# Performance work log

Hardware: AMD Instinct MI355X
Metric: run time of the kernel (lower is better)

Reference implementation:

```python
import jax, jax.numpy as jnp
import numpy as np

FP4_VALUES = jnp.array([0.0, 0.5, 1.0, 1.5, 2.0, 3.0, 4.0, 6.0,
                        -0.0, -0.5, -1.0, -1.5, -2.0, -3.0, -4.0, -6.0], dtype=jnp.float32)
ALPHA = 1.702
LIMIT = 7.0


def convert_moe_packed_tensors(blocks, scales):
    """Dequantize MXFP4: blocks [E, R, G, 16] packed nibbles, scales [E, R, G] biased exponents.
    Returns [E, G*32, R] fp32 (transposed like the torch reference)."""
    lo = FP4_VALUES[blocks & 0x0F]          # even output positions
    hi = FP4_VALUES[(blocks >> 4) & 0x0F]   # odd output positions
    vals = jnp.stack([lo, hi], axis=-1).reshape(*blocks.shape[:-1], 32)  # [E,R,G,32] interleaved
    scale = jnp.exp2((scales - 127).astype(jnp.float32))                 # 2**(s-127)
    w = vals * scale[..., None]
    E, R = blocks.shape[0], blocks.shape[1]
    return w.reshape(E, R, -1).transpose(0, 2, 1)  # [E, G*32, R]


def setup_inputs() -> dict:
    key = jax.random.key(0)
    ks = jax.random.split(key, 8)
    E, H, I = 8, 2880, 2880
    B, S = 1, 1024
    hidden_states = jax.random.normal(ks[0], (B, S, H), dtype=jnp.float32)
    routing_weights = jax.random.uniform(ks[1], (B * S, E), dtype=jnp.float32)
    gate_up_proj_blocks = jax.random.randint(ks[2], (E, 2 * I, H // 32, 16), 0, 256, dtype=jnp.int32)
    gate_up_proj_scales = jax.random.randint(ks[3], (E, 2 * I, H // 32), 118, 130, dtype=jnp.int32)
    gate_up_proj_bias = jax.random.normal(ks[4], (E, 2 * I), dtype=jnp.float32)
    down_proj_blocks = jax.random.randint(ks[5], (E, H, I // 32, 16), 0, 256, dtype=jnp.int32)
    down_proj_scales = jax.random.randint(ks[6], (E, H, I // 32), 118, 130, dtype=jnp.int32)
    down_proj_bias = jax.random.normal(ks[7], (E, H), dtype=jnp.float32)
    return {
        "hidden_states": hidden_states,
        "routing_weights": routing_weights,
        "gate_up_proj_blocks": gate_up_proj_blocks,
        "gate_up_proj_scales": gate_up_proj_scales,
        "gate_up_proj_bias": gate_up_proj_bias,
        "down_proj_blocks": down_proj_blocks,
        "down_proj_scales": down_proj_scales,
        "down_proj_bias": down_proj_bias,
    }


def reference(hidden_states, routing_weights, gate_up_proj_blocks, gate_up_proj_scales,
              gate_up_proj_bias, down_proj_blocks, down_proj_scales, down_proj_bias):
    B, S, H = hidden_states.shape
    gate_up_proj = convert_moe_packed_tensors(gate_up_proj_blocks, gate_up_proj_scales)  # [E, H, 2I]
    down_proj = convert_moe_packed_tensors(down_proj_blocks, down_proj_scales)           # [E, I, H]
    x = hidden_states.reshape(-1, H)                                                     # [T, H]
    # dense all-expert GLU MLP
    gate_up = jnp.einsum('th,ehf->etf', x, gate_up_proj) + gate_up_proj_bias[:, None, :]  # [E, T, 2I]
    gate = jnp.minimum(gate_up[..., ::2], LIMIT)
    up = jnp.clip(gate_up[..., 1::2], -LIMIT, LIMIT)
    glu = gate * jax.nn.sigmoid(gate * ALPHA)
    nxt = jnp.einsum('eti,eih->eth', (up + 1.0) * glu, down_proj) + down_proj_bias[:, None, :]  # [E, T, H]
    nxt = nxt * routing_weights.T[:, :, None]   # weight each expert's output per token
    out = nxt.sum(axis=0).reshape(B, S, H)
    return out
```

## Files before the change

### kernel.cpp

```cpp
#include <hip/hip_runtime.h>
#include <cstdint>


typedef float  floatx4 __attribute__((ext_vector_type(4)));
typedef __bf16 bf16x8  __attribute__((ext_vector_type(8)));

#define E8   8
#define Hdim 2880
#define Idim 2880
#define Ttok 1024
#define R1   5760
#define Gg   90
#define K2   (E8 * Idim)

__device__ __forceinline__ void load_lds16(const void* gptr, void* lptr) {
  __builtin_amdgcn_global_load_lds(
      (const __attribute__((address_space(1))) uint32_t*)gptr,
      (__attribute__((address_space(3))) uint32_t*)lptr, 16, 0, 0);
}

__device__ __forceinline__ uint32_t f2bf(float f) {
  uint32_t u = __float_as_uint(f);
  return (u + 0x7FFFu + ((u >> 16) & 1u)) >> 16;
}

__device__ __forceinline__ uint32_t perm(uint32_t hi, uint32_t lo, uint32_t sel) {
  return __builtin_amdgcn_perm(hi, lo, sel);
}

struct DqLut { uint32_t Ll, Lh, Hl, Hh; };

__device__ __forceinline__ DqLut make_lut(int s) {
  uint32_t A  = ((uint32_t)(s - 127) << 7) & 0xFFFFu;
  uint32_t e1 = (0x3F00u + A) & 0xFFFFu, e2 = (0x3F80u + A) & 0xFFFFu;
  uint32_t e3 = (0x3FC0u + A) & 0xFFFFu, e4 = (0x4000u + A) & 0xFFFFu;
  uint32_t e5 = (0x4040u + A) & 0xFFFFu, e6 = (0x4080u + A) & 0xFFFFu;
  uint32_t e7 = (0x40C0u + A) & 0xFFFFu;
  uint32_t B01 = e1 << 16, B23 = e2 | (e3 << 16);
  uint32_t B45 = e4 | (e5 << 16), B67 = e6 | (e7 << 16);
  DqLut L;
  L.Ll = perm(B23, B01, 0x06040200u);
  L.Hl = perm(B23, B01, 0x07050301u);
  L.Lh = perm(B67, B45, 0x06040200u);
  L.Hh = perm(B67, B45, 0x07050301u);
  return L;
}

__device__ __forceinline__ uint4 dq8(const DqLut& L, int4 wr) {
  uint32_t p = perm((uint32_t)wr.y, (uint32_t)wr.x, 0x04000400u);
  uint32_t q = perm((uint32_t)wr.w, (uint32_t)wr.z, 0x04000400u);
  uint32_t w = perm(q, p, 0x05040100u);
  uint32_t ilo = w & 0x07070707u;
  uint32_t ihi = (w >> 4) & 0x07070707u;
  uint32_t Llo = perm(L.Lh, L.Ll, ilo);
  uint32_t Hlo = perm(L.Hh, L.Hl, ilo) | ((w << 4) & 0x80808080u);
  uint32_t Lhi = perm(L.Lh, L.Ll, ihi);
  uint32_t Hhi = perm(L.Hh, L.Hl, ihi) | (w & 0x80808080u);
  uint32_t t0 = perm(Hlo, Llo, 0x05010400u);
  uint32_t t1 = perm(Hlo, Llo, 0x07030602u);
  uint32_t t2 = perm(Hhi, Lhi, 0x05010400u);
  uint32_t t3 = perm(Hhi, Lhi, 0x07030602u);
  uint4 o;
  o.x = perm(t2, t0, 0x05040100u);
  o.y = perm(t2, t0, 0x07060302u);
  o.z = perm(t3, t1, 0x05040100u);
  o.w = perm(t3, t1, 0x07060302u);
  return o;
}

__global__ void cvt_x_kernel(const float* __restrict__ x, uint16_t* __restrict__ xb, int n) {
  int i = (blockIdx.x * 256 + threadIdx.x) * 4;
  if (i >= n) return;
  float4 v = *(const float4*)(x + i);
  ushort4 o = make_ushort4((uint16_t)f2bf(v.x), (uint16_t)f2bf(v.y),
                           (uint16_t)f2bf(v.z), (uint16_t)f2bf(v.w));
  *(ushort4*)(xb + i) = o;
}

__global__ void dq_w_kernel(const int* __restrict__ blocks, const int* __restrict__ scales,
                            uint16_t* __restrict__ wd) {
  size_t g = (size_t)blockIdx.x * 256 + threadIdx.x;
  const int4* bp = (const int4*)(blocks + g * 16);
  int4 w0 = bp[0], w1 = bp[1], w2 = bp[2], w3 = bp[3];
  DqLut L = make_lut(scales[g]);
  uint4* op = (uint4*)(wd + g * 32);
  op[0] = dq8(L, w0); op[1] = dq8(L, w1); op[2] = dq8(L, w2); op[3] = dq8(L, w3);
}

__global__ void dq_w2t_kernel(const int* __restrict__ blocks, const int* __restrict__ scales,
                              uint16_t* __restrict__ wt) {
  size_t g = (size_t)blockIdx.x * 256 + threadIdx.x;
  int e  = (int)(g / ((size_t)Hdim * Gg));
  int rm = (int)(g % ((size_t)Hdim * Gg));
  int h  = rm / Gg;
  int ig = rm % Gg;
  const int4* bp = (const int4*)(blocks + g * 16);
  int4 w0 = bp[0], w1 = bp[1], w2 = bp[2], w3 = bp[3];
  DqLut L = make_lut(scales[g]);
  uint4* op = (uint4*)(wt + ((size_t)h * E8 + e) * Idim + (size_t)ig * 32);
  op[0] = dq8(L, w0); op[1] = dq8(L, w1); op[2] = dq8(L, w2); op[3] = dq8(L, w3);
}

__global__ void bias_init_kernel(const float* __restrict__ rw, const float* __restrict__ bias,
                                 float* __restrict__ out) {
  int t  = blockIdx.y;
  int h4 = (blockIdx.x * 256 + threadIdx.x) * 4;
  if (h4 >= Hdim) return;
  float4 s = make_float4(0.f, 0.f, 0.f, 0.f);
  #pragma unroll
  for (int e = 0; e < E8; ++e) {
    float w = rw[t * E8 + e];
    float4 b = *(const float4*)(bias + (size_t)e * Hdim + h4);
    s.x += w * b.x; s.y += w * b.y; s.z += w * b.z; s.w += w * b.w;
  }
  *(float4*)(out + (size_t)t * Hdim + h4) = s;
}

__global__ __launch_bounds__(256) void gemm1_pd_kernel(
    const uint16_t* __restrict__ xb, const uint16_t* __restrict__ w1d,
    const float* __restrict__ bias, const float* __restrict__ rw,
    uint16_t* __restrict__ act) {
  __shared__ uint16_t sA[128 * 64];
  __shared__ uint16_t sB[128 * 64];
  const int tid  = threadIdx.x;
  const int lane = tid & 63, wv = tid >> 6;
  const int wx = wv & 1, wy = wv >> 1;
  const int col = lane & 15, quad = lane >> 4;
  const int e  = blockIdx.z;
  const int t0 = blockIdx.x * 128;
  const int i0 = blockIdx.y * 64;

  floatx4 acc[4][4] = {};

  const uint16_t* aSrc[4];
  const uint16_t* bSrc[4];
  uint16_t* aDst[4];
  uint16_t* bDst[4];
  #pragma unroll
  for (int q = 0; q < 4; ++q) {
    int L = wv * 256 + q * 64 + lane;
    int row = L >> 3;
    int c = (L & 7) ^ (row & 7);
    aSrc[q] = xb + (size_t)(t0 + row) * Hdim + c * 8;
    aDst[q] = &sA[(size_t)(wv * 256 + q * 64) * 8];
    int orig = 2 * (((row >> 6) << 5) + (row & 31)) + ((row >> 5) & 1);
    bSrc[q] = w1d + ((size_t)e * R1 + 2 * i0 + orig) * Hdim + c * 8;
    bDst[q] = &sB[(size_t)(wv * 256 + q * 64) * 8];
  }

  for (int kt = 0; kt < 45; ++kt) {
    __syncthreads();
    const int k0 = kt * 64;
    #pragma unroll
    for (int q = 0; q < 4; ++q) load_lds16(aSrc[q] + k0, aDst[q]);
    #pragma unroll
    for (int q = 0; q < 4; ++q) load_lds16(bSrc[q] + k0, bDst[q]);
    __syncthreads();
    #pragma unroll
    for (int ks = 0; ks < 2; ++ks) {
      bf16x8 af[4], bfr[4];
      #pragma unroll
      for (int fm = 0; fm < 4; ++fm) {
        int row = wy * 64 + fm * 16 + col;
        int c = ((ks << 2) | quad) ^ (row & 7);
        af[fm] = *(const bf16x8*)&sA[row * 64 + c * 8];
      }
      #pragma unroll
      for (int fn = 0; fn < 4; ++fn) {
        int row = wx * 64 + fn * 16 + col;
        int c = ((ks << 2) | quad) ^ (row & 7);
        bfr[fn] = *(const bf16x8*)&sB[row * 64 + c * 8];
      }
      #pragma unroll
      for (int fm = 0; fm < 4; ++fm)
        #pragma unroll
        for (int fn = 0; fn < 4; ++fn)
          acc[fm][fn] = __builtin_amdgcn_mfma_f32_16x16x32_bf16(
              af[fm], bfr[fn], acc[fm][fn], 0, 0, 0);
    }
  }

  #pragma unroll
  for (int fm = 0; fm < 4; ++fm) {
    #pragma unroll
    for (int p = 0; p < 2; ++p) {
      floatx4 ga = acc[fm][p], ua = acc[fm][p + 2];
      int ig = i0 + wx * 32 + p * 16 + col;
      float bg = bias[(size_t)e * R1 + 2 * ig];
      float bu = bias[(size_t)e * R1 + 2 * ig + 1];
      #pragma unroll
      for (int r = 0; r < 4; ++r) {
        int t = t0 + wy * 64 + fm * 16 + quad * 4 + r;
        float gate = fminf(ga[r] + bg, 7.0f);
        float up   = fminf(fmaxf(ua[r] + bu, -7.0f), 7.0f);
        float glu  = gate / (1.0f + __expf(-1.702f * gate));
        float a    = rw[t * E8 + e] * (up + 1.0f) * glu;
        act[((size_t)t * E8 + e) * Idim + ig] = (uint16_t)f2bf(a);
      }
    }
  }
}

__global__ __launch_bounds__(256) void gemm2_ks_kernel(
    const uint16_t* __restrict__ actT, const uint16_t* __restrict__ w2t,
    float* __restrict__ out) {
  __shared__ uint16_t sA[128 * 64];
  __shared__ uint16_t sB[96 * 64];
  const int tid  = threadIdx.x;
  const int lane = tid & 63, wv = tid >> 6;
  const int wx = wv & 1, wy = wv >> 1;
  const int col = lane & 15, quad = lane >> 4;
  const int t0 = blockIdx.x * 128;
  const int h0 = blockIdx.y * 96;
  const int kbase = blockIdx.z * (K2 / 2);

  floatx4 acc[4][3] = {};

  const uint16_t* aSrc[4];
  uint16_t* aDst[4];
  #pragma unroll
  for (int q = 0; q < 4; ++q) {
    int L = wv * 256 + q * 64 + lane;
    int row = L >> 3;
    int c = (L & 7) ^ (row & 7);
    aSrc[q] = actT + (size_t)(t0 + row) * K2 + kbase + c * 8;
    aDst[q] = &sA[(size_t)(wv * 256 + q * 64) * 8];
  }
  const uint16_t* bSrc[3];
  uint16_t* bDst[3];
  #pragma unroll
  for (int q = 0; q < 3; ++q) {
    int L = wv * 192 + q * 64 + lane;
    int row = L >> 3;
    int c = (L & 7) ^ (row & 7);
    bSrc[q] = w2t + (size_t)(h0 + row) * K2 + kbase + c * 8;
    bDst[q] = &sB[(size_t)(wv * 192 + q * 64) * 8];
  }

  for (int kt = 0; kt < 180; ++kt) {
    __syncthreads();
    const int k0 = kt * 64;
    #pragma unroll
    for (int q = 0; q < 4; ++q) load_lds16(aSrc[q] + k0, aDst[q]);
    #pragma unroll
    for (int q = 0; q < 3; ++q) load_lds16(bSrc[q] + k0, bDst[q]);
    __syncthreads();
    #pragma unroll
    for (int ks = 0; ks < 2; ++ks) {
      bf16x8 af[4], bfr[3];
      #pragma unroll
      for (int fm = 0; fm < 4; ++fm) {
        int row = wy * 64 + fm * 16 + col;
        int c = ((ks << 2) | quad) ^ (row & 7);
        af[fm] = *(const bf16x8*)&sA[row * 64 + c * 8];
      }
      #pragma unroll
      for (int fn = 0; fn < 3; ++fn) {
        int row = wx * 48 + fn * 16 + col;
        int c = ((ks << 2) | quad) ^ (row & 7);
        bfr[fn] = *(const bf16x8*)&sB[row * 64 + c * 8];
      }
      #pragma unroll
      for (int fm = 0; fm < 4; ++fm)
        #pragma unroll
        for (int fn = 0; fn < 3; ++fn)
          acc[fm][fn] = __builtin_amdgcn_mfma_f32_16x16x32_bf16(
              af[fm], bfr[fn], acc[fm][fn], 0, 0, 0);
    }
  }

  #pragma unroll
  for (int fm = 0; fm < 4; ++fm)
    #pragma unroll
    for (int fn = 0; fn < 3; ++fn) {
      int h = h0 + wx * 48 + fn * 16 + col;
      #pragma unroll
      for (int r = 0; r < 4; ++r) {
        int t = t0 + wy * 64 + fm * 16 + quad * 4 + r;
        atomicAdd(out + (size_t)t * Hdim + h, acc[fm][fn][r]);
      }
    }
}

extern "C" void kernel_launch(void* const* d_in, const int* in_sizes, int n_in,
                              void* d_out, int out_size, void* d_ws, size_t ws_size,
                              hipStream_t stream) {
  (void)in_sizes; (void)n_in; (void)out_size; (void)ws_size;
  const float* x        = (const float*)d_in[0];
  const float* rw       = (const float*)d_in[1];
  const int*   gub_b    = (const int*)d_in[2];
  const int*   gub_s    = (const int*)d_in[3];
  const float* gub_bias = (const float*)d_in[4];
  const int*   dwn_b    = (const int*)d_in[5];
  const int*   dwn_s    = (const int*)d_in[6];
  const float* dwn_bias = (const float*)d_in[7];
  float* out = (float*)d_out;

  const size_t nXb  = (size_t)Ttok * Hdim;
  const size_t nAct = (size_t)Ttok * K2;
  const size_t nW1  = (size_t)E8 * R1 * Hdim;

  uint16_t* xb  = (uint16_t*)d_ws;
  uint16_t* act = xb + nXb;
  uint16_t* w1d = act + nAct;
  uint16_t* w2t = w1d + nW1;

  cvt_x_kernel<<<dim3((Ttok * Hdim / 4 + 255) / 256), 256, 0, stream>>>(x, xb, Ttok * Hdim);
  dq_w_kernel<<<dim3((int)((size_t)E8 * R1 * Gg / 256)), 256, 0, stream>>>(gub_b, gub_s, w1d);
  dq_w2t_kernel<<<dim3((int)((size_t)E8 * Hdim * Gg / 256)), 256, 0, stream>>>(dwn_b, dwn_s, w2t);
  bias_init_kernel<<<dim3(3, Ttok), 256, 0, stream>>>(rw, dwn_bias, out);
  gemm1_pd_kernel<<<dim3(8, 45, 8), 256, 0, stream>>>(xb, w1d, gub_bias, rw, act);
  gemm2_ks_kernel<<<dim3(8, 30, 2), 256, 0, stream>>>(act, w2t, out);
}
```

Measured before the change: 1.187 ms.

## Triple-buffer gemm1 with async LDS loads and widen gemm2 split-K

```diff
diff --git a/kernel.cpp b/kernel.cpp
--- a/kernel.cpp
+++ b/kernel.cpp
@@ -116,68 +116,89 @@
   *(float4*)(out + (size_t)t * Hdim + h4) = s;
 }
 
-__global__ __launch_bounds__(256) void gemm1_pd_kernel(
+__global__ __launch_bounds__(512) void gemm1_dp_kernel(
     const uint16_t* __restrict__ xb, const uint16_t* __restrict__ w1d,
     const float* __restrict__ bias, const float* __restrict__ rw,
     uint16_t* __restrict__ act) {
-  __shared__ uint16_t sA[128 * 64];
-  __shared__ uint16_t sB[128 * 64];
+  extern __shared__ uint16_t smem[];
+  uint16_t* sAr = smem;
+  uint16_t* sBr = smem + 3 * 8192;
   const int tid  = threadIdx.x;
   const int lane = tid & 63, wv = tid >> 6;
-  const int wx = wv & 1, wy = wv >> 1;
+  const int wm = wv >> 1, wn = wv & 1;
   const int col = lane & 15, quad = lane >> 4;
   const int e  = blockIdx.z;
-  const int t0 = blockIdx.x * 128;
+  const int t0 = blockIdx.x * 256;
   const int i0 = blockIdx.y * 64;
 
   floatx4 acc[4][4] = {};
 
-  const uint16_t* aSrc[4];
-  const uint16_t* bSrc[4];
-  uint16_t* aDst[4];
-  uint16_t* bDst[4];
-  #pragma unroll
-  for (int q = 0; q < 4; ++q) {
-    int L = wv * 256 + q * 64 + lane;
-    int row = L >> 3;
-    int c = (L & 7) ^ (row & 7);
-    aSrc[q] = xb + (size_t)(t0 + row) * Hdim + c * 8;
-    aDst[q] = &sA[(size_t)(wv * 256 + q * 64) * 8];
-    int orig = 2 * (((row >> 6) << 5) + (row & 31)) + ((row >> 5) & 1);
-    bSrc[q] = w1d + ((size_t)e * R1 + 2 * i0 + orig) * Hdim + c * 8;
-    bDst[q] = &sB[(size_t)(wv * 256 + q * 64) * 8];
-  }
-
-  for (int kt = 0; kt < 45; ++kt) {
-    __syncthreads();
-    const int k0 = kt * 64;
-    #pragma unroll
-    for (int q = 0; q < 4; ++q) load_lds16(aSrc[q] + k0, aDst[q]);
-    #pragma unroll
-    for (int q = 0; q < 4; ++q) load_lds16(bSrc[q] + k0, bDst[q]);
-    __syncthreads();
-    #pragma unroll
-    for (int ks = 0; ks < 2; ++ks) {
-      bf16x8 af[4], bfr[4];
-      #pragma unroll
-      for (int fm = 0; fm < 4; ++fm) {
-        int row = wy * 64 + fm * 16 + col;
-        int c = ((ks << 2) | quad) ^ (row & 7);
-        af[fm] = *(const bf16x8*)&sA[row * 64 + c * 8];
-      }
-      #pragma unroll
-      for (int fn = 0; fn < 4; ++fn) {
-        int row = wx * 64 + fn * 16 + col;
-        int c = ((ks << 2) | quad) ^ (row & 7);
-        bfr[fn] = *(const bf16x8*)&sB[row * 64 + c * 8];
-      }
-      #pragma unroll
-      for (int fm = 0; fm < 4; ++fm)
-        #pragma unroll
-        for (int fn = 0; fn < 4; ++fn)
-          acc[fm][fn] = __builtin_amdgcn_mfma_f32_16x16x32_bf16(
-              af[fm], bfr[fn], acc[fm][fn], 0, 0, 0);
-    }
+  const uint16_t* aSrc0;
+  const uint16_t* aSrc1;
+  const uint16_t* bSrc;
+  {
+    int L0 = tid;
+    int r0 = L0 >> 2;
+    int g0 = (L0 & 3) ^ ((r0 >> 1) & 3);
+    aSrc0 = xb + (size_t)(t0 + r0) * Hdim + g0 * 8;
+    int L1 = 512 + tid;
+    int r1 = L1 >> 2;
+    int g1 = (L1 & 3) ^ ((r1 >> 1) & 3);
+    aSrc1 = xb + (size_t)(t0 + r1) * Hdim + g1 * 8;
+    int rb = tid >> 2;
+    int gb = (tid & 3) ^ ((rb >> 1) & 3);
+    int orig = 2 * (((rb >> 6) << 5) + (rb & 31)) + ((rb >> 5) & 1);
+    bSrc = w1d + ((size_t)e * R1 + 2 * i0 + orig) * Hdim + gb * 8;
+  }
+  const int aOff0 = (wv * 64) * 8;
+  const int aOff1 = (512 + wv * 64) * 8;
+  const int bOff  = (wv * 64) * 8;
+
+  auto STAGE = [&](int kt, int slot) {
+    const int k0 = kt * 32;
+    uint16_t* A = sAr + slot * 8192;
+    uint16_t* B = sBr + slot * 4096;
+    load_lds16(aSrc0 + k0, A + aOff0);
+    load_lds16(aSrc1 + k0, A + aOff1);
+    load_lds16(bSrc + k0, B + bOff);
+  };
+
+  STAGE(0, 0);
+  STAGE(1, 1);
+
+  int sr = 0;
+  for (int j = 0; j < 90; ++j) {
+    asm volatile("s_waitcnt vmcnt(3)" ::: "memory");
+    __builtin_amdgcn_s_barrier();
+    asm volatile("" ::: "memory");
+    int js = j + 2; if (js > 89) js = 89;
+    int sw = sr + 2; if (sw >= 3) sw -= 3;
+    STAGE(js, sw);
+
+    const uint16_t* A = sAr + sr * 8192;
+    const uint16_t* B = sBr + sr * 4096;
+    bf16x8 af[4], bfr[4];
+    #pragma unroll
+    for (int fm = 0; fm < 4; ++fm) {
+      int row = wm * 64 + fm * 16 + col;
+      int g = quad ^ ((row >> 1) & 3);
+      af[fm] = *(const bf16x8*)&A[row * 32 + g * 8];
+    }
+    #pragma unroll
+    for (int fn = 0; fn < 4; ++fn) {
+      int row = wn * 64 + fn * 16 + col;
+      int g = quad ^ ((row >> 1) & 3);
+      bfr[fn] = *(const bf16x8*)&B[row * 32 + g * 8];
+    }
+    __builtin_amdgcn_s_setprio(1);
+    #pragma unroll
+    for (int fm = 0; fm < 4; ++fm)
+      #pragma unroll
+      for (int fn = 0; fn < 4; ++fn)
+        acc[fm][fn] = __builtin_amdgcn_mfma_f32_16x16x32_bf16(
+            af[fm], bfr[fn], acc[fm][fn], 0, 0, 0);
+    __builtin_amdgcn_s_setprio(0);
+    sr = (sr + 1 == 3) ? 0 : sr + 1;
   }
 
   #pragma unroll
@@ -185,12 +206,12 @@
     #pragma unroll
     for (int p = 0; p < 2; ++p) {
       floatx4 ga = acc[fm][p], ua = acc[fm][p + 2];
-      int ig = i0 + wx * 32 + p * 16 + col;
+      int ig = i0 + wn * 32 + p * 16 + col;
       float bg = bias[(size_t)e * R1 + 2 * ig];
       float bu = bias[(size_t)e * R1 + 2 * ig + 1];
       #pragma unroll
       for (int r = 0; r < 4; ++r) {
-        int t = t0 + wy * 64 + fm * 16 + quad * 4 + r;
+        int t = t0 + wm * 64 + fm * 16 + quad * 4 + r;
         float gate = fminf(ga[r] + bg, 7.0f);
         float up   = fminf(fmaxf(ua[r] + bu, -7.0f), 7.0f);
         float glu  = gate / (1.0f + __expf(-1.702f * gate));
@@ -212,7 +233,7 @@
   const int col = lane & 15, quad = lane >> 4;
   const int t0 = blockIdx.x * 128;
   const int h0 = blockIdx.y * 96;
-  const int kbase = blockIdx.z * (K2 / 2);
+  const int kbase = blockIdx.z * (K2 / 4);
 
   floatx4 acc[4][3] = {};
 
@@ -237,7 +258,7 @@
     bDst[q] = &sB[(size_t)(wv * 192 + q * 64) * 8];
   }
 
-  for (int kt = 0; kt < 180; ++kt) {
+  for (int kt = 0; kt < 90; ++kt) {
     __syncthreads();
     const int k0 = kt * 64;
     #pragma unroll
@@ -305,10 +326,17 @@
   uint16_t* w1d = act + nAct;
   uint16_t* w2t = w1d + nW1;
 
+  static int attr_set = 0;
+  if (!attr_set) {
+    (void)hipFuncSetAttribute((const void*)gemm1_dp_kernel,
+                              hipFuncAttributeMaxDynamicSharedMemorySize, 73728);
+    attr_set = 1;
+  }
+
   cvt_x_kernel<<<dim3((Ttok * Hdim / 4 + 255) / 256), 256, 0, stream>>>(x, xb, Ttok * Hdim);
   dq_w_kernel<<<dim3((int)((size_t)E8 * R1 * Gg / 256)), 256, 0, stream>>>(gub_b, gub_s, w1d);
   dq_w2t_kernel<<<dim3((int)((size_t)E8 * Hdim * Gg / 256)), 256, 0, stream>>>(dwn_b, dwn_s, w2t);
   bias_init_kernel<<<dim3(3, Ttok), 256, 0, stream>>>(rw, dwn_bias, out);
-  gemm1_pd_kernel<<<dim3(8, 45, 8), 256, 0, stream>>>(xb, w1d, gub_bias, rw, act);
-  gemm2_ks_kernel<<<dim3(8, 30, 2), 256, 0, stream>>>(act, w2t, out);
-}
+  gemm1_dp_kernel<<<dim3(4, 45, 8), 512, 73728, stream>>>(xb, w1d, gub_bias, rw, act);
+  gemm2_ks_kernel<<<dim3(8, 30, 4), 256, 0, stream>>>(act, w2t, out);
+}
```

Measured after the change: 1.082 ms. 1.1x faster.
